# Kernel tuning notes

Measured on AMD Instinct MI355X. Metric: run time of the kernel, lower is better.

## Reference

```python
import jax, jax.numpy as jnp
import numpy as np

EMB_DIM = 1024
NUM_HEADS = 16
SCALE_WEIGHTS = 1.0
TINY = jnp.finfo(jnp.float32).tiny


def setup_inputs() -> dict:
    key = jax.random.key(0)
    k1, k2, k3 = jax.random.split(key, 3)
    B, S = 2, 2048
    x = jax.random.normal(k1, (B, S, EMB_DIM), dtype=jnp.float32)
    weights = jax.random.uniform(k2, (B, S), dtype=jnp.float32)
    W_qkv = jax.random.normal(k3, (EMB_DIM, 3 * EMB_DIM), dtype=jnp.float32) / np.sqrt(EMB_DIM)
    b_qkv = jnp.zeros((3 * EMB_DIM,), dtype=jnp.float32)
    return {"x": x, "weights": weights, "W_qkv": W_qkv, "b_qkv": b_qkv}


def reference(x, weights, W_qkv, b_qkv):
    B, S, E = x.shape
    H = NUM_HEADS
    hd = E // H
    # QKV projection: [B,S,3E] -> [B,H,S,3*hd] -> split
    qkv = x @ W_qkv + b_qkv
    qkv = qkv.reshape(B, S, H, 3 * hd).transpose(0, 2, 1, 3)
    q, k, v = jnp.split(qkv, 3, axis=-1)  # each [B,H,S,hd]
    # weights: [B,S] -> [B,1,1,S] (broadcast over heads and query positions)
    w = weights[:, None, None, :]
    # scores with log-weight bias and hard masks
    attn_logits = jnp.einsum("bhqd,bhkd->bhqk", q, k) / jnp.sqrt(jnp.asarray(hd, x.dtype))
    attn_logits = attn_logits + jnp.log(w / SCALE_WEIGHTS + TINY)
    attn_logits = jnp.where(w == 0, -9e15, attn_logits)
    attn_logits = jnp.where(w == 1, 9e15, attn_logits)
    attention = jax.nn.softmax(attn_logits, axis=-1)
    values = jnp.einsum("bhqk,bhkd->bhqd", attention, v)
    return values.transpose(0, 2, 1, 3).reshape(B, S, E)
```

## Files before the change

### kernel.cpp

```cpp
#include <hip/hip_runtime.h>
#include <math.h>

#define B_  2
#define S_  2048
#define E_  1024
#define H_  16
#define HD_ 64
#define N3_ 3072
#define M_  (B_*S_)

typedef _Float16 h8  __attribute__((ext_vector_type(8)));
typedef _Float16 h4  __attribute__((ext_vector_type(4)));
typedef float    f4  __attribute__((ext_vector_type(4)));
typedef float    fv16 __attribute__((ext_vector_type(16)));

typedef __attribute__((address_space(3))) unsigned int       lds_u32;
typedef const __attribute__((address_space(1))) unsigned int glob_u32;

__device__ __forceinline__ void gld16(const void* g, void* l) {
    __builtin_amdgcn_global_load_lds((glob_u32*)g, (lds_u32*)l, 16, 0, 0);
}
__device__ __forceinline__ float exp2_hw(float x) { return __builtin_amdgcn_exp2f(x); }

#define QSCALE 0.18033688011112042f

__global__ void cvt_x_kernel(const float* __restrict__ x, _Float16* __restrict__ x16) {
    int i = (blockIdx.x * 256 + threadIdx.x) * 8;
    float4 u = *(const float4*)&x[i];
    float4 v = *(const float4*)&x[i + 4];
    h8 o;
    o[0] = (_Float16)u.x; o[1] = (_Float16)u.y; o[2] = (_Float16)u.z; o[3] = (_Float16)u.w;
    o[4] = (_Float16)v.x; o[5] = (_Float16)v.y; o[6] = (_Float16)v.z; o[7] = (_Float16)v.w;
    *(h8*)&x16[i] = o;
}

__global__ __launch_bounds__(256) void transpose_w_kernel(
        const float* __restrict__ W, _Float16* __restrict__ Wt) {
    __shared__ float T[64][65];
    int k0 = blockIdx.x * 64, n0 = blockIdx.y * 64;
    int tid = threadIdx.x;
    int r = tid >> 4, c4 = (tid & 15) * 4;
#pragma unroll
    for (int i = 0; i < 4; i++) {
        int row = r + i * 16;
        float4 u = *(const float4*)&W[(size_t)(k0 + row) * N3_ + n0 + c4];
        T[c4 + 0][row] = u.x; T[c4 + 1][row] = u.y;
        T[c4 + 2][row] = u.z; T[c4 + 3][row] = u.w;
    }
    __syncthreads();
#pragma unroll
    for (int i = 0; i < 4; i++) {
        int rn = r + i * 16;
        h4 p;
        p[0] = (_Float16)T[rn][c4 + 0]; p[1] = (_Float16)T[rn][c4 + 1];
        p[2] = (_Float16)T[rn][c4 + 2]; p[3] = (_Float16)T[rn][c4 + 3];
        *(h4*)&Wt[(size_t)(n0 + rn) * E_ + k0 + c4] = p;
    }
}

__global__ __launch_bounds__(256, 2) void qkv_gemm32(
        const _Float16* __restrict__ x16, const _Float16* __restrict__ wt,
        const float* __restrict__ bq, const float* __restrict__ w,
        _Float16* __restrict__ qws, _Float16* __restrict__ kws,
        _Float16* __restrict__ vtws) {
    __shared__ __align__(16) _Float16 Ab[2][128 * 64];
    __shared__ __align__(16) _Float16 Wb[2][192 * 64];

    int tid = threadIdx.x;
    int wid = tid >> 6, lane = tid & 63;
    int l31 = lane & 31, hi = lane >> 5, l7 = l31 & 7;
    int srow = lane >> 3;
    int wm = wid & 1, wn = wid >> 1;

    int L = blockIdx.x;
    int head = 2 * (L & 7) + (L >> 8);
    int mb = (L >> 3) & 31;
    int m0 = mb * 128;
    int n0 = head * 192;
    int b = m0 >> 11;
    int bh = b * H_ + head;
    int sblk = m0 & 2047;

    fv16 acc[2][3];
#pragma unroll
    for (int ntl = 0; ntl < 3; ntl++) {
        int n_abs = wn * 96 + ntl * 32;
        int which = n_abs >> 6;
        fv16 ini;
        if (which == 2) {
            float bb = bq[n0 + n_abs + l31];
#pragma unroll
            for (int r = 0; r < 16; r++) ini[r] = bb;
        } else {
#pragma unroll
            for (int g = 0; g < 4; g++) {
                f4 bv = *(const f4*)&bq[n0 + n_abs + 8 * g + 4 * hi];
#pragma unroll
                for (int j = 0; j < 4; j++) ini[4 * g + j] = bv[j];
            }
        }
        acc[0][ntl] = ini; acc[1][ntl] = ini;
    }

    auto stage = [&](int t, int bf) {
        int k0 = t * 64;
#pragma unroll
        for (int j = 0; j < 4; j++) {
            int batch = wid * 4 + j;
            int row = batch * 8 + srow;
            int ch = (lane & 7) ^ srow ^ (batch & 7);
            gld16(&x16[(size_t)(m0 + row) * E_ + k0 + ch * 8], &Ab[bf][batch * 8 * 64]);
        }
#pragma unroll
        for (int j = 0; j < 6; j++) {
            int batch = wid * 6 + j;
            int row = batch * 8 + srow;
            int ch = (lane & 7) ^ srow ^ (batch & 7);
            gld16(&wt[(size_t)(n0 + row) * E_ + k0 + ch * 8], &Wb[bf][batch * 8 * 64]);
        }
    };

    stage(0, 0);

    for (int t = 0; t < 16; t++) {
        int bf = t & 1;
        __syncthreads();
        if (t < 15) stage(t + 1, bf ^ 1);
#pragma unroll
        for (int step = 0; step < 4; step++) {
            h8 af[2], wf[3];
#pragma unroll
            for (int mt = 0; mt < 2; mt++) {
                int R = wm * 64 + mt * 32 + l31;
                int ph = ((2 * step + hi) ^ l7 ^ ((mt * 4 + (l31 >> 3)) & 7)) * 8;
                af[mt] = *(const h8*)&Ab[bf][R * 64 + ph];
            }
#pragma unroll
            for (int ntl = 0; ntl < 3; ntl++) {
                int R = wn * 96 + ntl * 32 + l31;
                int ph = ((2 * step + hi) ^ l7 ^ ((wn * 12 + ntl * 4 + (l31 >> 3)) & 7)) * 8;
                wf[ntl] = *(const h8*)&Wb[bf][R * 64 + ph];
            }
#pragma unroll
            for (int ntl = 0; ntl < 3; ntl++) {
                bool isv = (wn == 1) && (ntl >= 1);
#pragma unroll
                for (int mt = 0; mt < 2; mt++) {
                    if (isv)
                        acc[mt][ntl] = __builtin_amdgcn_mfma_f32_32x32x16_f16(af[mt], wf[ntl], acc[mt][ntl], 0, 0, 0);
                    else
                        acc[mt][ntl] = __builtin_amdgcn_mfma_f32_32x32x16_f16(wf[ntl], af[mt], acc[mt][ntl], 0, 0, 0);
                }
            }
        }
    }

#pragma unroll
    for (int ntl = 0; ntl < 3; ntl++) {
        int n_abs = wn * 96 + ntl * 32;
        int which = n_abs >> 6;
#pragma unroll
        for (int mt = 0; mt < 2; mt++) {
            if (which == 2) {
                int d = (n_abs & 63) + l31;
#pragma unroll
                for (int g = 0; g < 4; g++) {
                    int soff = wm * 64 + mt * 32 + 8 * g + 4 * hi;
                    f4 wf4 = *(const f4*)&w[m0 + soff];
                    h4 p;
#pragma unroll
                    for (int j = 0; j < 4; j++)
                        p[j] = (_Float16)(acc[mt][ntl][4 * g + j] * wf4[j]);
                    *(h4*)&vtws[((size_t)bh * 64 + d) * S_ + sblk + soff] = p;
                }
            } else {
                _Float16* dst = (which == 0) ? qws : kws;
                float scale = (which == 0) ? QSCALE : 1.0f;
                int s = sblk + wm * 64 + mt * 32 + l31;
#pragma unroll
                for (int g = 0; g < 4; g++) {
                    int d0 = (n_abs & 63) + 8 * g + 4 * hi;
                    h4 p;
#pragma unroll
                    for (int j = 0; j < 4; j++)
                        p[j] = (_Float16)(acc[mt][ntl][4 * g + j] * scale);
                    *(h4*)&dst[((size_t)bh * S_ + s) * 64 + d0] = p;
                }
            }
        }
    }
}

__global__ __launch_bounds__(256, 2) void attn_kernel(
        const _Float16* __restrict__ q, const _Float16* __restrict__ k,
        const _Float16* __restrict__ vt, const float* __restrict__ w,
        float* __restrict__ out) {
    __shared__ __align__(16) _Float16 Kb[2][64 * 64];
    __shared__ __align__(16) _Float16 Vb[2][64 * 64];
    __shared__ __align__(16) float lws[2048];

    int tid = threadIdx.x;
    int wid = tid >> 6, lane = tid & 63;
    int l31 = lane & 31, hi = lane >> 5, l7 = l31 & 7;
    int srow = lane >> 3;
    int L = blockIdx.x;
    int bh = (L & 7) + 8 * (L >> 7);
    int qt = (L >> 3) & 15;
    int q0 = qt * 128;
    int b = bh >> 4, h = bh & 15;

    const _Float16* qbase = q + (size_t)bh * S_ * HD_;
    const _Float16* kbase = k + (size_t)bh * S_ * HD_;
    const _Float16* vbase = vt + (size_t)bh * HD_ * S_;
    const float* wbase = w + (size_t)b * S_;

#pragma unroll
    for (int j = 0; j < 2; j++) {
        int batch = wid + 4 * j;
        gld16(&wbase[batch * 256 + lane * 4], &lws[batch * 256]);
    }

    auto stage = [&](int kt, int bf) {
        int k0 = kt * 64;
#pragma unroll
        for (int j = 0; j < 2; j++) {
            int batch = wid * 2 + j;
            int row = batch * 8 + srow;
            int ch = (lane & 7) ^ srow ^ (batch & 7);
            gld16(&kbase[(size_t)(k0 + row) * 64 + ch * 8], &Kb[bf][batch * 8 * 64]);
            gld16(&vbase[(size_t)row * S_ + k0 + ch * 8], &Vb[bf][batch * 8 * 64]);
        }
    };

    stage(0, 0);

    int qrow = q0 + wid * 32 + l31;
    h8 qf[4];
#pragma unroll
    for (int step = 0; step < 4; step++)
        qf[step] = *(const h8*)&qbase[(size_t)qrow * 64 + 16 * step + 8 * hi];

    fv16 o[2];
    o[0] = (fv16)0.0f; o[1] = (fv16)0.0f;
    float m_r = -INFINITY, l_r = 0.0f;

    for (int kt = 0; kt < 32; kt++) {
        int bf = kt & 1;
        __syncthreads();
        if (kt < 31) stage(kt + 1, bf ^ 1);

        fv16 st[2];
        st[0] = (fv16)0.0f; st[1] = (fv16)0.0f;
#pragma unroll
        for (int step = 0; step < 4; step++) {
#pragma unroll
            for (int kt2 = 0; kt2 < 2; kt2++) {
                int R = kt2 * 32 + l31;
                int ph = ((2 * step + hi) ^ l7 ^ ((kt2 * 4 + (l31 >> 3)) & 7)) * 8;
                h8 kf = *(const h8*)&Kb[bf][R * 64 + ph];
                st[kt2] = __builtin_amdgcn_mfma_f32_32x32x16_f16(kf, qf[step], st[kt2], 0, 0, 0);
            }
        }

        float rm = -INFINITY;
#pragma unroll
        for (int kt2 = 0; kt2 < 2; kt2++)
#pragma unroll
            for (int r = 0; r < 16; r++) rm = fmaxf(rm, st[kt2][r]);
        rm = fmaxf(rm, __shfl_xor(rm, 32));
        float mnew = fmaxf(m_r, rm);
        float rs = 0.0f;
        h4 pf[2][4];
        int k0 = kt * 64;
#pragma unroll
        for (int kt2 = 0; kt2 < 2; kt2++)
#pragma unroll
            for (int g = 0; g < 4; g++) {
                f4 wv = *(const f4*)&lws[k0 + kt2 * 32 + 8 * g + 4 * hi];
                f4 e;
#pragma unroll
                for (int j = 0; j < 4; j++) {
                    float ev = exp2_hw(st[kt2][4 * g + j] - mnew);
                    e[j] = ev;
                    rs += ev * wv[j];
                }
                h4 p;
                p[0] = (_Float16)e[0]; p[1] = (_Float16)e[1];
                p[2] = (_Float16)e[2]; p[3] = (_Float16)e[3];
                pf[kt2][g] = p;
            }
        rs += __shfl_xor(rs, 32);
        float alpha = exp2_hw(m_r - mnew);
        m_r = mnew;
        l_r = l_r * alpha + rs;
        o[0] = o[0] * alpha;
        o[1] = o[1] * alpha;

#pragma unroll
        for (int kt2 = 0; kt2 < 2; kt2++)
#pragma unroll
            for (int g = 0; g < 4; g++) {
                int c = 4 * kt2 + g;
#pragma unroll
                for (int dt = 0; dt < 2; dt++) {
                    int R = dt * 32 + l31;
                    int ph = (c ^ l7 ^ ((dt * 4 + (l31 >> 3)) & 7)) * 8 + hi * 4;
                    h4 vf = *(const h4*)&Vb[bf][R * 64 + ph];
                    o[dt] = __builtin_amdgcn_mfma_f32_32x32x8f16(vf, pf[kt2][g], o[dt], 0, 0, 0);
                }
            }
    }

    float linv = 1.0f / l_r;
    float* obase = &out[((size_t)(b * S_ + qrow)) * E_ + h * 64];
#pragma unroll
    for (int dt = 0; dt < 2; dt++)
#pragma unroll
        for (int g = 0; g < 4; g++) {
            int d0 = dt * 32 + 8 * g + 4 * hi;
            f4 ov;
#pragma unroll
            for (int j = 0; j < 4; j++) ov[j] = o[dt][4 * g + j] * linv;
            *(f4*)&obase[d0] = ov;
        }
}

extern "C" void kernel_launch(void* const* d_in, const int* in_sizes, int n_in,
                              void* d_out, int out_size, void* d_ws, size_t ws_size,
                              hipStream_t stream) {
    const float* x  = (const float*)d_in[0];
    const float* w  = (const float*)d_in[1];
    const float* Wq = (const float*)d_in[2];
    const float* bq = (const float*)d_in[3];
    float* out = (float*)d_out;

    char* p = (char*)d_ws;
    _Float16* x16 = (_Float16*)p;              p += (size_t)M_ * E_ * 2;
    _Float16* wt  = (_Float16*)p;              p += (size_t)E_ * N3_ * 2;
    _Float16* qb  = (_Float16*)p;              p += (size_t)M_ * E_ * 2;
    _Float16* kb  = (_Float16*)p;              p += (size_t)M_ * E_ * 2;
    _Float16* vtb = (_Float16*)p;

    cvt_x_kernel<<<dim3(M_ * E_ / 2048), dim3(256), 0, stream>>>(x, x16);
    transpose_w_kernel<<<dim3(E_ / 64, N3_ / 64), dim3(256), 0, stream>>>(Wq, wt);
    qkv_gemm32<<<dim3(512), dim3(256), 0, stream>>>(x16, wt, bq, w, qb, kb, vtb);
    attn_kernel<<<dim3(512), dim3(256), 0, stream>>>(qb, kb, vtb, w, out);
}
```

Measured before the change: 179.5 us.

## Split attention over key halves with flash-decoding combine kernel

The attention kernel now splits the key dimension into two halves, launching twice as many blocks. Each block writes a normalized fp16 partial output plus its running max and sum, and a new combine kernel merges the two halves into the fp32 output. This raises the block count from 512 to 1024 so more waves can keep the MI355X's CUs busy, at the cost of an extra kernel launch, partial-result traffic and fp16 rounding of the partials. Float-to-half conversions are also switched to packed round-toward-zero cvt_pkrtz instructions.

Result: no change. 182.2 us (+1.5%).

```diff
diff --git a/kernel.cpp b/kernel.cpp
--- a/kernel.cpp
+++ b/kernel.cpp
@@ -8,9 +8,11 @@
 #define HD_ 64
 #define N3_ 3072
 #define M_  (B_*S_)
+#define NROWS_ (32 * S_)
 
 typedef _Float16 h8  __attribute__((ext_vector_type(8)));
 typedef _Float16 h4  __attribute__((ext_vector_type(4)));
+typedef __fp16   fp16v2 __attribute__((ext_vector_type(2)));
 typedef float    f4  __attribute__((ext_vector_type(4)));
 typedef float    fv16 __attribute__((ext_vector_type(16)));
 
@@ -21,6 +23,12 @@
     __builtin_amdgcn_global_load_lds((glob_u32*)g, (lds_u32*)l, 16, 0, 0);
 }
 __device__ __forceinline__ float exp2_hw(float x) { return __builtin_amdgcn_exp2f(x); }
+__device__ __forceinline__ h4 pack4(float a, float b, float c, float d) {
+    union { struct { fp16v2 l, h; } p; h4 v; } u;
+    u.p.l = __builtin_amdgcn_cvt_pkrtz(a, b);
+    u.p.h = __builtin_amdgcn_cvt_pkrtz(c, d);
+    return u.v;
+}
 
 #define QSCALE 0.18033688011112042f
 
@@ -167,10 +175,10 @@
                 for (int g = 0; g < 4; g++) {
                     int soff = wm * 64 + mt * 32 + 8 * g + 4 * hi;
                     f4 wf4 = *(const f4*)&w[m0 + soff];
-                    h4 p;
-#pragma unroll
-                    for (int j = 0; j < 4; j++)
-                        p[j] = (_Float16)(acc[mt][ntl][4 * g + j] * wf4[j]);
+                    h4 p = pack4(acc[mt][ntl][4 * g + 0] * wf4[0],
+                                 acc[mt][ntl][4 * g + 1] * wf4[1],
+                                 acc[mt][ntl][4 * g + 2] * wf4[2],
+                                 acc[mt][ntl][4 * g + 3] * wf4[3]);
                     *(h4*)&vtws[((size_t)bh * 64 + d) * S_ + sblk + soff] = p;
                 }
             } else {
@@ -180,10 +188,10 @@
 #pragma unroll
                 for (int g = 0; g < 4; g++) {
                     int d0 = (n_abs & 63) + 8 * g + 4 * hi;
-                    h4 p;
-#pragma unroll
-                    for (int j = 0; j < 4; j++)
-                        p[j] = (_Float16)(acc[mt][ntl][4 * g + j] * scale);
+                    h4 p = pack4(acc[mt][ntl][4 * g + 0] * scale,
+                                 acc[mt][ntl][4 * g + 1] * scale,
+                                 acc[mt][ntl][4 * g + 2] * scale,
+                                 acc[mt][ntl][4 * g + 3] * scale);
                     *(h4*)&dst[((size_t)bh * S_ + s) * 64 + d0] = p;
                 }
             }
@@ -194,34 +202,32 @@
 __global__ __launch_bounds__(256, 2) void attn_kernel(
         const _Float16* __restrict__ q, const _Float16* __restrict__ k,
         const _Float16* __restrict__ vt, const float* __restrict__ w,
-        float* __restrict__ out) {
+        _Float16* __restrict__ opart, float* __restrict__ ml) {
     __shared__ __align__(16) _Float16 Kb[2][64 * 64];
     __shared__ __align__(16) _Float16 Vb[2][64 * 64];
-    __shared__ __align__(16) float lws[2048];
+    __shared__ __align__(16) float lws[1024];
 
     int tid = threadIdx.x;
     int wid = tid >> 6, lane = tid & 63;
     int l31 = lane & 31, hi = lane >> 5, l7 = l31 & 7;
     int srow = lane >> 3;
     int L = blockIdx.x;
-    int bh = (L & 7) + 8 * (L >> 7);
+    int bh = (L & 7) + 8 * (L >> 8);
     int qt = (L >> 3) & 15;
+    int half = (L >> 7) & 1;
     int q0 = qt * 128;
-    int b = bh >> 4, h = bh & 15;
+    int kh0 = half * 1024;
+    int b = bh >> 4;
 
     const _Float16* qbase = q + (size_t)bh * S_ * HD_;
     const _Float16* kbase = k + (size_t)bh * S_ * HD_;
     const _Float16* vbase = vt + (size_t)bh * HD_ * S_;
     const float* wbase = w + (size_t)b * S_;
 
-#pragma unroll
-    for (int j = 0; j < 2; j++) {
-        int batch = wid + 4 * j;
-        gld16(&wbase[batch * 256 + lane * 4], &lws[batch * 256]);
-    }
+    gld16(&wbase[kh0 + wid * 256 + lane * 4], &lws[wid * 256]);
 
     auto stage = [&](int kt, int bf) {
-        int k0 = kt * 64;
+        int k0 = kh0 + kt * 64;
 #pragma unroll
         for (int j = 0; j < 2; j++) {
             int batch = wid * 2 + j;
@@ -244,10 +250,10 @@
     o[0] = (fv16)0.0f; o[1] = (fv16)0.0f;
     float m_r = -INFINITY, l_r = 0.0f;
 
-    for (int kt = 0; kt < 32; kt++) {
+    for (int kt = 0; kt < 16; kt++) {
         int bf = kt & 1;
         __syncthreads();
-        if (kt < 31) stage(kt + 1, bf ^ 1);
+        if (kt < 15) stage(kt + 1, bf ^ 1);
 
         fv16 st[2];
         st[0] = (fv16)0.0f; st[1] = (fv16)0.0f;
@@ -271,23 +277,19 @@
         float mnew = fmaxf(m_r, rm);
         float rs = 0.0f;
         h4 pf[2][4];
-        int k0 = kt * 64;
+        int kk = kt * 64;
 #pragma unroll
         for (int kt2 = 0; kt2 < 2; kt2++)
 #pragma unroll
             for (int g = 0; g < 4; g++) {
-                f4 wv = *(const f4*)&lws[k0 + kt2 * 32 + 8 * g + 4 * hi];
-                f4 e;
-#pragma unroll
-                for (int j = 0; j < 4; j++) {
-                    float ev = exp2_hw(st[kt2][4 * g + j] - mnew);
-                    e[j] = ev;
-                    rs += ev * wv[j];
-                }
-                h4 p;
-                p[0] = (_Float16)e[0]; p[1] = (_Float16)e[1];
-                p[2] = (_Float16)e[2]; p[3] = (_Float16)e[3];
-                pf[kt2][g] = p;
+                f4 wv = *(const f4*)&lws[kk + kt2 * 32 + 8 * g + 4 * hi];
+                float e0 = exp2_hw(st[kt2][4 * g + 0] - mnew);
+                float e1 = exp2_hw(st[kt2][4 * g + 1] - mnew);
+                float e2 = exp2_hw(st[kt2][4 * g + 2] - mnew);
+                float e3 = exp2_hw(st[kt2][4 * g + 3] - mnew);
+                rs = fmaf(e0, wv[0], rs); rs = fmaf(e1, wv[1], rs);
+                rs = fmaf(e2, wv[2], rs); rs = fmaf(e3, wv[3], rs);
+                pf[kt2][g] = pack4(e0, e1, e2, e3);
             }
         rs += __shfl_xor(rs, 32);
         float alpha = exp2_hw(m_r - mnew);
@@ -311,18 +313,54 @@
             }
     }
 
+    size_t prow = (size_t)(half * 32 + bh) * S_ + qrow;
     float linv = 1.0f / l_r;
-    float* obase = &out[((size_t)(b * S_ + qrow)) * E_ + h * 64];
+    _Float16* obase = &opart[prow * 64];
 #pragma unroll
     for (int dt = 0; dt < 2; dt++)
 #pragma unroll
         for (int g = 0; g < 4; g++) {
             int d0 = dt * 32 + 8 * g + 4 * hi;
-            f4 ov;
-#pragma unroll
-            for (int j = 0; j < 4; j++) ov[j] = o[dt][4 * g + j] * linv;
-            *(f4*)&obase[d0] = ov;
-        }
+            h4 p = pack4(o[dt][4 * g + 0] * linv, o[dt][4 * g + 1] * linv,
+                         o[dt][4 * g + 2] * linv, o[dt][4 * g + 3] * linv);
+            *(h4*)&obase[d0] = p;
+        }
+    if (hi == 0) {
+        float2 v; v.x = m_r; v.y = l_r;
+        *(float2*)&ml[prow * 2] = v;
+    }
+}
+
+__global__ __launch_bounds__(256) void combine_kernel(
+        const _Float16* __restrict__ opart, const float* __restrict__ ml,
+        float* __restrict__ out) {
+    int t = threadIdx.x;
+    int r = blockIdx.x * 64 + (t >> 2);
+    int dg = (t & 3) * 16;
+    int bh = r >> 11, qrow = r & 2047;
+    float2 ml0 = *(const float2*)&ml[(size_t)r * 2];
+    float2 ml1 = *(const float2*)&ml[((size_t)NROWS_ + r) * 2];
+    float Mx = fmaxf(ml0.x, ml1.x);
+    float w0 = ml0.y * exp2_hw(ml0.x - Mx);
+    float w1 = ml1.y * exp2_hw(ml1.x - Mx);
+    float inv = 1.0f / (w0 + w1);
+    w0 *= inv; w1 *= inv;
+    const _Float16* o0 = &opart[(size_t)r * 64 + dg];
+    const _Float16* o1 = &opart[((size_t)NROWS_ + r) * 64 + dg];
+    float* ob = &out[((size_t)((bh >> 4) * S_ + qrow)) * E_ + (bh & 15) * 64 + dg];
+#pragma unroll
+    for (int i = 0; i < 2; i++) {
+        h8 a = *(const h8*)&o0[i * 8];
+        h8 c = *(const h8*)&o1[i * 8];
+        f4 r0, r1;
+#pragma unroll
+        for (int j = 0; j < 4; j++) {
+            r0[j] = (float)a[j] * w0 + (float)c[j] * w1;
+            r1[j] = (float)a[4 + j] * w0 + (float)c[4 + j] * w1;
+        }
+        *(f4*)&ob[i * 8] = r0;
+        *(f4*)&ob[i * 8 + 4] = r1;
+    }
 }
 
 extern "C" void kernel_launch(void* const* d_in, const int* in_sizes, int n_in,
@@ -339,10 +377,13 @@
     _Float16* wt  = (_Float16*)p;              p += (size_t)E_ * N3_ * 2;
     _Float16* qb  = (_Float16*)p;              p += (size_t)M_ * E_ * 2;
     _Float16* kb  = (_Float16*)p;              p += (size_t)M_ * E_ * 2;
-    _Float16* vtb = (_Float16*)p;
+    _Float16* vtb = (_Float16*)p;              p += (size_t)M_ * E_ * 2;
+    _Float16* opart = (_Float16*)p;            p += (size_t)2 * NROWS_ * 64 * 2;
+    float* mlb = (float*)p;
 
     cvt_x_kernel<<<dim3(M_ * E_ / 2048), dim3(256), 0, stream>>>(x, x16);
     transpose_w_kernel<<<dim3(E_ / 64, N3_ / 64), dim3(256), 0, stream>>>(Wq, wt);
     qkv_gemm32<<<dim3(512), dim3(256), 0, stream>>>(x16, wt, bq, w, qb, kb, vtb);
-    attn_kernel<<<dim3(512), dim3(256), 0, stream>>>(qb, kb, vtb, w, out);
-}
+    attn_kernel<<<dim3(1024), dim3(256), 0, stream>>>(qb, kb, vtb, w, opart, mlb);
+    combine_kernel<<<dim3(NROWS_ / 64), dim3(256), 0, stream>>>(opart, mlb, out);
+}
```
